# Performance work log

Hardware: AMD Instinct MI355X
Metric: run time of the kernel (lower is better)

Reference implementation:

```python
import jax, jax.numpy as jnp
import numpy as np

SEQ_LEN = 2048
EMBED = 1024
HIDDEN = 64
BATCH = 8


def setup_inputs() -> dict:
    key = jax.random.key(0)
    ks = jax.random.split(key, 7)
    s = 1.0 / np.sqrt(EMBED)
    return {
        "inputs": jax.random.normal(ks[0], (BATCH, SEQ_LEN, EMBED), dtype=jnp.float32),
        "Wq": jax.random.uniform(ks[1], (EMBED, HIDDEN), jnp.float32, -s, s),
        "bq": jax.random.uniform(ks[2], (HIDDEN,), jnp.float32, -s, s),
        "Wk": jax.random.uniform(ks[3], (EMBED, HIDDEN), jnp.float32, -s, s),
        "bk": jax.random.uniform(ks[4], (HIDDEN,), jnp.float32, -s, s),
        "Wv": jax.random.uniform(ks[5], (EMBED, HIDDEN), jnp.float32, -s, s),
        "bv": jax.random.uniform(ks[6], (HIDDEN,), jnp.float32, -s, s),
    }


def reference(inputs, Wq, bq, Wk, bk, Wv, bv):
    # inputs: [B, T, E]
    q = inputs @ Wq + bq  # [B, T, H]
    k = inputs @ Wk + bk
    v = inputs @ Wv + bv
    scale = 1.0 / jnp.sqrt(jnp.asarray(k.shape[-1], q.dtype))
    scores = jnp.einsum("bqh,bkh->bqk", q, k) * scale  # [B, T, T]
    T = scores.shape[1]
    tril = jnp.tril(jnp.ones((T, T), dtype=scores.dtype))
    # NOTE: multiplicative mask (zeros out future scores) exactly as in the torch module,
    # NOT an additive -inf mask.
    scores = scores * tril
    attn = jax.nn.softmax(scores, axis=-1)
    return jnp.einsum("bqk,bkh->bqh", attn, v)  # [B, T, H]
```

## Files before the change

### kernel.cpp

```cpp
#include <hip/hip_runtime.h>

#define NBATCH 8
#define TSEQ 2048
#define EDIM 1024
#define HDIM 64
#define NROW (NBATCH * TSEQ)

typedef unsigned short u16;
typedef __attribute__((ext_vector_type(8))) short bf16x8;
typedef __attribute__((ext_vector_type(8))) short short8;
typedef __attribute__((ext_vector_type(4))) float f32x4;

typedef unsigned int uint_as1 __attribute__((address_space(1)));
typedef unsigned int uint_as3 __attribute__((address_space(3)));

__device__ __forceinline__ u16 f2b(float x) {
  unsigned int u = __float_as_uint(x);
  unsigned int r = (u + 0x7fffu + ((u >> 16) & 1u)) >> 16;
  return (u16)r;
}
__device__ __forceinline__ float b2f(u16 h) {
  return __uint_as_float(((unsigned int)h) << 16);
}
__device__ __forceinline__ void gl16(const void* g, void* l) {
  __builtin_amdgcn_global_load_lds((const uint_as1*)g, (uint_as3*)l, 16, 0, 0);
}

__global__ __launch_bounds__(256) void wt_kernel(
    const float* __restrict__ Wq, const float* __restrict__ Wk,
    const float* __restrict__ Wv, u16* __restrict__ Wt) {
  __shared__ float s[64][65];
  const int o = blockIdx.x >> 4, et = blockIdx.x & 15;
  const float* W = (o == 0) ? Wq : (o == 1) ? Wk : Wv;
  const int t = threadIdx.x;
  const int e0 = et * 64;
#pragma unroll
  for (int i = 0; i < 16; i++) {
    int e = i * 4 + (t >> 6), h = t & 63;
    s[e][h] = W[(size_t)(e0 + e) * HDIM + h];
  }
  __syncthreads();
#pragma unroll
  for (int j = 0; j < 16; j++) {
    int h = j * 4 + (t >> 6), e = t & 63;
    Wt[(size_t)(o * 64 + h) * EDIM + e0 + e] = f2b(s[e][h]);
  }
}

#define XBUF (32 * 256)
#define WBUF (192 * 128)

__global__ __launch_bounds__(256, 2) void proj_mfma(
    const float* __restrict__ X, const u16* __restrict__ Wt,
    const float* __restrict__ bq, const float* __restrict__ bk,
    const float* __restrict__ bv,
    u16* __restrict__ Qb, u16* __restrict__ Kb, u16* __restrict__ Vt) {
  __shared__ __align__(16) char sx[2 * XBUF];
  __shared__ __align__(16) char sw[2 * WBUF];

  const int tid = threadIdx.x;
  const int w = tid >> 6, l = tid & 63;
  const int g = l >> 4, li = l & 15;
  const long bt0 = (long)blockIdx.x * 32;

  const int xr = tid >> 4, xc = tid & 15;
  const float* xsrc0 = X + (bt0 + xr) * EDIM + ((xc ^ (xr & 7)) * 4);
  const float* xsrc1 = X + (bt0 + 16 + xr) * EDIM + ((xc ^ (xr & 7)) * 4);

  f32x4 acc[6];
#pragma unroll
  for (int i = 0; i < 6; i++) acc[i] = (f32x4)0.f;

#define STAGE(BUF, E0)                                                       \
  do {                                                                       \
    gl16(xsrc0 + (E0), sx + (BUF)*XBUF + tid * 16);                          \
    gl16(xsrc1 + (E0), sx + (BUF)*XBUF + (tid + 256) * 16);                  \
    _Pragma("unroll") for (int j = 0; j < 6; j++) {                          \
      const int L = j * 256 + tid;                                           \
      const int r = L >> 3, c = L & 7;                                       \
      gl16(Wt + (size_t)r * EDIM + (E0) + ((c ^ (r & 7)) * 8),               \
           sw + (BUF)*WBUF + L * 16);                                        \
    }                                                                        \
  } while (0)

  STAGE(0, 0);
  asm volatile("s_waitcnt vmcnt(0)" ::: "memory");
  __builtin_amdgcn_sched_barrier(0);
  __builtin_amdgcn_s_barrier();
  __builtin_amdgcn_sched_barrier(0);

  for (int ks = 0; ks < 16; ks++) {
    const int buf = ks & 1;
    if (ks < 15) STAGE(buf ^ 1, (ks + 1) * 64);
    __builtin_amdgcn_sched_barrier(0);
    if (ks < 15) {
      asm volatile("s_waitcnt vmcnt(8)" ::: "memory");
    } else {
      asm volatile("s_waitcnt vmcnt(0)" ::: "memory");
    }
    __builtin_amdgcn_sched_barrier(0);
    __builtin_amdgcn_s_barrier();
    __builtin_amdgcn_sched_barrier(0);

    const char* xb = sx + buf * XBUF;
    const char* wb = sw + buf * WBUF;
    bf16x8 bfr[2][2];
#pragma unroll
    for (int cs = 0; cs < 2; cs++) {
      const int row = cs * 16 + li;
#pragma unroll
      for (int kc = 0; kc < 2; kc++) {
        const int G0 = kc * 8 + g * 2;
        const float4 f0 = *(const float4*)(xb + row * 256 + ((G0 ^ (row & 7)) * 16));
        const float4 f1 = *(const float4*)(xb + row * 256 + (((G0 + 1) ^ (row & 7)) * 16));
        bfr[cs][kc] = (bf16x8){(short)f2b(f0.x), (short)f2b(f0.y),
                               (short)f2b(f0.z), (short)f2b(f0.w),
                               (short)f2b(f1.x), (short)f2b(f1.y),
                               (short)f2b(f1.z), (short)f2b(f1.w)};
      }
    }
#pragma unroll
    for (int mt = 0; mt < 3; mt++) {
      const int row = w * 48 + mt * 16 + li;
#pragma unroll
      for (int kc = 0; kc < 2; kc++) {
        const int G = kc * 4 + g;
        const bf16x8 af = *(const bf16x8*)(wb + row * 128 + ((G ^ (row & 7)) * 16));
        acc[mt * 2 + 0] = __builtin_amdgcn_mfma_f32_16x16x32_bf16(
            af, bfr[0][kc], acc[mt * 2 + 0], 0, 0, 0);
        acc[mt * 2 + 1] = __builtin_amdgcn_mfma_f32_16x16x32_bf16(
            af, bfr[1][kc], acc[mt * 2 + 1], 0, 0, 0);
      }
    }
    __builtin_amdgcn_sched_barrier(0);
    __builtin_amdgcn_s_barrier();
    __builtin_amdgcn_sched_barrier(0);
  }
#undef STAGE

  const float qscale = 0.18033688011112042f;
#pragma unroll
  for (int cs = 0; cs < 2; cs++) {
    const long tg = bt0 + cs * 16 + li;
    const int b = (int)(tg >> 11), tl = (int)(tg & 2047);
#pragma unroll
    for (int mt = 0; mt < 3; mt++) {
      const int n0 = w * 48 + mt * 16 + g * 4;
      const int o = n0 >> 6;
      const int h0 = n0 & 63;
      const float* bias = (o == 0) ? bq : (o == 1) ? bk : bv;
      const float4 bb = *(const float4*)&bias[h0];
      const f32x4 a = acc[mt * 2 + cs];
      float v0 = a.x + bb.x, v1 = a.y + bb.y;
      float v2 = a.z + bb.z, v3 = a.w + bb.w;
      if (o == 0) {
        v0 *= qscale; v1 *= qscale; v2 *= qscale; v3 *= qscale;
        uint2 pk = make_uint2((unsigned)f2b(v0) | ((unsigned)f2b(v1) << 16),
                              (unsigned)f2b(v2) | ((unsigned)f2b(v3) << 16));
        *(uint2*)&Qb[tg * HDIM + h0] = pk;
      } else if (o == 1) {
        uint2 pk = make_uint2((unsigned)f2b(v0) | ((unsigned)f2b(v1) << 16),
                              (unsigned)f2b(v2) | ((unsigned)f2b(v3) << 16));
        *(uint2*)&Kb[tg * HDIM + h0] = pk;
      } else {
        Vt[(size_t)(b * 64 + h0 + 0) * TSEQ + tl] = f2b(v0);
        Vt[(size_t)(b * 64 + h0 + 1) * TSEQ + tl] = f2b(v1);
        Vt[(size_t)(b * 64 + h0 + 2) * TSEQ + tl] = f2b(v2);
        Vt[(size_t)(b * 64 + h0 + 3) * TSEQ + tl] = f2b(v3);
      }
    }
  }
}

__global__ __launch_bounds__(1024) void css_kernel(const u16* __restrict__ Vt,
                                                   float* __restrict__ CSS) {
  __shared__ float cs[32][64];
  const int b = blockIdx.x;
  const int t = threadIdx.x;
  const int h = t & 63, cg = t >> 6;
  const u16* vp = Vt + ((size_t)b * 64 + h) * TSEQ + cg * 128;
  float s0 = 0.f, s1 = 0.f;
#pragma unroll
  for (int i = 0; i < 8; i++) {
    const short8 a = *(const short8*)(vp + i * 8);
    s0 += b2f((u16)a[0]) + b2f((u16)a[1]) + b2f((u16)a[2]) + b2f((u16)a[3]) +
          b2f((u16)a[4]) + b2f((u16)a[5]) + b2f((u16)a[6]) + b2f((u16)a[7]);
  }
#pragma unroll
  for (int i = 8; i < 16; i++) {
    const short8 a = *(const short8*)(vp + i * 8);
    s1 += b2f((u16)a[0]) + b2f((u16)a[1]) + b2f((u16)a[2]) + b2f((u16)a[3]) +
          b2f((u16)a[4]) + b2f((u16)a[5]) + b2f((u16)a[6]) + b2f((u16)a[7]);
  }
  cs[cg * 2 + 0][h] = s0;
  cs[cg * 2 + 1][h] = s1;
  __syncthreads();
  if (t < 64) {
    float S = 0.f;
    CSS[((size_t)b * 33 + 32) * 64 + t] = 0.f;
    for (int c = 31; c >= 0; c--) {
      S += cs[c][t];
      CSS[((size_t)b * 33 + c) * 64 + t] = S;
    }
  }
}

#define ISSUE_K(K0A, K1A, KO)                                              \
  do {                                                                     \
    _Pragma("unroll") for (int n = 0; n < 4; n++) {                        \
      const u16* kp_ = Kbb + (size_t)((KO) + n * 16 + li) * HDIM + g * 8;  \
      K0A[n] = *(const bf16x8*)(kp_);                                      \
      K1A[n] = *(const bf16x8*)(kp_ + 32);                                 \
    }                                                                      \
  } while (0)

#define ISSUE_V(KO)                                                        \
  do {                                                                     \
    _Pragma("unroll") for (int n = 0; n < 4; n++) {                        \
      const u16* vp_ = Vtb + (size_t)(n * 16 + li) * TSEQ + (KO) + g * 8;  \
      vf0[n] = *(const bf16x8*)(vp_);                                      \
      vf1[n] = *(const bf16x8*)(vp_ + 32);                                 \
    }                                                                      \
  } while (0)

#define COMPUTE_TILE(K0A, K1A, KO)                                         \
  do {                                                                     \
    f32x4 sA_[4], sB_[4];                                                  \
    __builtin_amdgcn_s_setprio(1);                                         \
    _Pragma("unroll") for (int n = 0; n < 4; n++) {                        \
      sA_[n] = (f32x4)0.f;                                                 \
      sA_[n] = __builtin_amdgcn_mfma_f32_16x16x32_bf16(K0A[n], qa0[0], sA_[n], 0, 0, 0); \
      sA_[n] = __builtin_amdgcn_mfma_f32_16x16x32_bf16(K1A[n], qa0[1], sA_[n], 0, 0, 0); \
      sB_[n] = (f32x4)0.f;                                                 \
      sB_[n] = __builtin_amdgcn_mfma_f32_16x16x32_bf16(K0A[n], qa1[0], sB_[n], 0, 0, 0); \
      sB_[n] = __builtin_amdgcn_mfma_f32_16x16x32_bf16(K1A[n], qa1[1], sB_[n], 0, 0, 0); \
    }                                                                      \
    __builtin_amdgcn_s_setprio(0);                                         \
    _Pragma("unroll") for (int n = 0; n < 4; n++) {                        \
      const int kb_ = (KO) + n * 16 + g * 4;                               \
      float p0_ = (kb_ + 0 <= qiL0) ? exp2f(sA_[n][0]) : 1.0f;             \
      float p1_ = (kb_ + 1 <= qiL0) ? exp2f(sA_[n][1]) : 1.0f;             \
      float p2_ = (kb_ + 2 <= qiL0) ? exp2f(sA_[n][2]) : 1.0f;             \
      float p3_ = (kb_ + 3 <= qiL0) ? exp2f(sA_[n][3]) : 1.0f;             \
      zaccA += (p0_ + p1_) + (p2_ + p3_);                                  \
      uint2 pk_ = make_uint2((unsigned)f2b(p0_) | ((unsigned)f2b(p1_) << 16), \
                             (unsigned)f2b(p2_) | ((unsigned)f2b(p3_) << 16)); \
      *(uint2*)(sppw + li * 144 + n * 32 + g * 8) = pk_;                   \
      float q0_ = (kb_ + 0 <= qiL1) ? exp2f(sB_[n][0]) : 1.0f;             \
      float q1_ = (kb_ + 1 <= qiL1) ? exp2f(sB_[n][1]) : 1.0f;             \
      float q2_ = (kb_ + 2 <= qiL1) ? exp2f(sB_[n][2]) : 1.0f;             \
      float q3_ = (kb_ + 3 <= qiL1) ? exp2f(sB_[n][3]) : 1.0f;             \
      zaccB += (q0_ + q1_) + (q2_ + q3_);                                  \
      uint2 qk_ = make_uint2((unsigned)f2b(q0_) | ((unsigned)f2b(q1_) << 16), \
                             (unsigned)f2b(q2_) | ((unsigned)f2b(q3_) << 16)); \
      *(uint2*)(sppw + (li + 16) * 144 + n * 32 + g * 8) = qk_;            \
    }                                                                      \
    asm volatile("s_waitcnt lgkmcnt(0)" ::: "memory");                     \
    __builtin_amdgcn_sched_barrier(0);                                     \
    const bf16x8 paA0_ = *(const bf16x8*)(sppw + li * 144 + g * 16);       \
    const bf16x8 paA1_ = *(const bf16x8*)(sppw + li * 144 + 64 + g * 16);  \
    const bf16x8 paB0_ = *(const bf16x8*)(sppw + (li + 16) * 144 + g * 16);\
    const bf16x8 paB1_ = *(const bf16x8*)(sppw + (li + 16) * 144 + 64 + g * 16); \
    __builtin_amdgcn_s_setprio(1);                                         \
    _Pragma("unroll") for (int nt = 0; nt < 4; nt++) {                     \
      oaccA[nt] = __builtin_amdgcn_mfma_f32_16x16x32_bf16(paA0_, vf0[nt], oaccA[nt], 0, 0, 0); \
      oaccA[nt] = __builtin_amdgcn_mfma_f32_16x16x32_bf16(paA1_, vf1[nt], oaccA[nt], 0, 0, 0); \
      oaccB[nt] = __builtin_amdgcn_mfma_f32_16x16x32_bf16(paB0_, vf0[nt], oaccB[nt], 0, 0, 0); \
      oaccB[nt] = __builtin_amdgcn_mfma_f32_16x16x32_bf16(paB1_, vf1[nt], oaccB[nt], 0, 0, 0); \
    }                                                                      \
    __builtin_amdgcn_s_setprio(0);                                         \
  } while (0)

__global__ __launch_bounds__(256, 2) void attn_mfma(
    const u16* __restrict__ Qb, const u16* __restrict__ Kb,
    const u16* __restrict__ Vt, const float* __restrict__ CSS,
    float* __restrict__ Out) {
  __shared__ __align__(16) u16 spp[4][32][72];
  __shared__ float spm[4][32][68];

  const int tid = threadIdx.x;
  const int w = tid >> 6, l = tid & 63;
  const int g = l >> 4, li = l & 15;

  const int gb = blockIdx.x & 7;
  const int j = blockIdx.x >> 3;
  const int gr = 63 - j;
  const int q0 = gr * 32;
  const int qiL0 = q0 + li;
  const int qiL1 = q0 + 16 + li;

  char* sppw = (char*)&spp[w][0][0];

  const size_t qbase0 = ((size_t)gb * TSEQ + q0 + li) * HDIM;
  bf16x8 qa0[2], qa1[2];
  qa0[0] = *(const bf16x8*)(Qb + qbase0 + g * 8);
  qa0[1] = *(const bf16x8*)(Qb + qbase0 + g * 8 + 32);
  qa1[0] = *(const bf16x8*)(Qb + qbase0 + 16 * HDIM + g * 8);
  qa1[1] = *(const bf16x8*)(Qb + qbase0 + 16 * HDIM + g * 8 + 32);

  float zaccA = 0.f, zaccB = 0.f;
  f32x4 oaccA[4], oaccB[4];
#pragma unroll
  for (int nt = 0; nt < 4; nt++) { oaccA[nt] = (f32x4)0.f; oaccB[nt] = (f32x4)0.f; }

  const int nt = gr / 2 + 1;
  const u16* Kbb = Kb + (size_t)gb * TSEQ * HDIM;
  const u16* Vtb = Vt + (size_t)gb * 64 * TSEQ;

  bf16x8 kA0[4], kA1[4], kB0[4], kB1[4], vf0[4], vf1[4];

  int kt = w;
  if (kt < nt) {
    ISSUE_K(kA0, kA1, kt * 64);
    while (true) {
      ISSUE_V(kt * 64);
      if (kt + 4 < nt) ISSUE_K(kB0, kB1, (kt + 4) * 64);
      __builtin_amdgcn_sched_barrier(0);
      COMPUTE_TILE(kA0, kA1, kt * 64);
      kt += 4;
      if (kt >= nt) break;
      ISSUE_V(kt * 64);
      if (kt + 4 < nt) ISSUE_K(kA0, kA1, (kt + 4) * 64);
      __builtin_amdgcn_sched_barrier(0);
      COMPUTE_TILE(kB0, kB1, kt * 64);
      kt += 4;
      if (kt >= nt) break;
    }
  }

  zaccA += __shfl_xor(zaccA, 16, 64);
  zaccA += __shfl_xor(zaccA, 32, 64);
  zaccB += __shfl_xor(zaccB, 16, 64);
  zaccB += __shfl_xor(zaccB, 32, 64);

#pragma unroll
  for (int n = 0; n < 4; n++) {
#pragma unroll
    for (int r = 0; r < 4; r++) {
      spm[w][g * 4 + r][n * 16 + li] = oaccA[n][r];
      spm[w][16 + g * 4 + r][n * 16 + li] = oaccB[n][r];
    }
  }
  if (l < 16) spm[w][l][64] = zaccA;
  else if (l < 32) spm[w][16 + (l & 15)][64] = zaccB;
  __syncthreads();

  const float tailz = (float)(TSEQ - nt * 64);
  const float tailv = CSS[((size_t)gb * 33 + nt) * 64 + l];
#pragma unroll
  for (int r = 0; r < 8; r++) {
    const int q = w * 8 + r;
    const int qi = q0 + q;
    float a = ((spm[0][q][l] + spm[1][q][l]) + (spm[2][q][l] + spm[3][q][l]));
    float zz = ((spm[0][q][64] + spm[1][q][64]) + (spm[2][q][64] + spm[3][q][64]));
    zz += tailz;
    a += tailv;
    Out[((size_t)gb * TSEQ + qi) * HDIM + l] = a / zz;
  }
}

extern "C" void kernel_launch(void* const* d_in, const int* in_sizes, int n_in,
                              void* d_out, int out_size, void* d_ws, size_t ws_size,
                              hipStream_t stream) {
  const float* X  = (const float*)d_in[0];
  const float* Wq = (const float*)d_in[1];
  const float* bq = (const float*)d_in[2];
  const float* Wk = (const float*)d_in[3];
  const float* bk = (const float*)d_in[4];
  const float* Wv = (const float*)d_in[5];
  const float* bv = (const float*)d_in[6];
  float* out = (float*)d_out;

  char* ws = (char*)d_ws;
  u16*   Qb  = (u16*)(ws);
  u16*   Kb  = (u16*)(ws + 2097152);
  u16*   Vt  = (u16*)(ws + 4194304);
  u16*   Wt  = (u16*)(ws + 6291456);
  float* CSS = (float*)(ws + 6684672);

  wt_kernel<<<48, 256, 0, stream>>>(Wq, Wk, Wv, Wt);
  proj_mfma<<<NROW / 32, 256, 0, stream>>>(X, Wt, bq, bk, bv, Qb, Kb, Vt);
  css_kernel<<<NBATCH, 1024, 0, stream>>>(Vt, CSS);
  attn_mfma<<<512, 256, 0, stream>>>(Qb, Kb, Vt, CSS, out);
}
```

Before: 69.71 us.

## Split projection kernel across Q/K/V outputs to triple grid parallelism

The projection kernel now launches three times as many blocks, and each block computes only one of the Q, K or V outputs (64 columns) for its 32-row tile. This shrinks the weight LDS buffer, the per-block accumulators and the number of loads per stage. The launch bound rises to 4 blocks per CU for higher occupancy. In exchange, each fp32 input tile is read from global memory three times and converted to bf16 three times, which triples the dominant X traffic unless L2 absorbs it.

```diff
diff --git a/kernel.cpp b/kernel.cpp
--- a/kernel.cpp
+++ b/kernel.cpp
@@ -48,9 +48,9 @@
 }
 
 #define XBUF (32 * 256)
-#define WBUF (192 * 128)
-
-__global__ __launch_bounds__(256, 2) void proj_mfma(
+#define WBUF (64 * 128)
+
+__global__ __launch_bounds__(256, 4) void proj_mfma(
     const float* __restrict__ X, const u16* __restrict__ Wt,
     const float* __restrict__ bq, const float* __restrict__ bk,
     const float* __restrict__ bv,
@@ -61,24 +61,26 @@
   const int tid = threadIdx.x;
   const int w = tid >> 6, l = tid & 63;
   const int g = l >> 4, li = l & 15;
-  const long bt0 = (long)blockIdx.x * 32;
+  const int o = blockIdx.x % 3;
+  const long bt0 = (long)(blockIdx.x / 3) * 32;
 
   const int xr = tid >> 4, xc = tid & 15;
   const float* xsrc0 = X + (bt0 + xr) * EDIM + ((xc ^ (xr & 7)) * 4);
   const float* xsrc1 = X + (bt0 + 16 + xr) * EDIM + ((xc ^ (xr & 7)) * 4);
-
-  f32x4 acc[6];
-#pragma unroll
-  for (int i = 0; i < 6; i++) acc[i] = (f32x4)0.f;
+  const u16* wsrc = Wt + (size_t)o * 64 * EDIM;
+
+  f32x4 acc[2];
+  acc[0] = (f32x4)0.f;
+  acc[1] = (f32x4)0.f;
 
 #define STAGE(BUF, E0)                                                       \
   do {                                                                       \
     gl16(xsrc0 + (E0), sx + (BUF)*XBUF + tid * 16);                          \
     gl16(xsrc1 + (E0), sx + (BUF)*XBUF + (tid + 256) * 16);                  \
-    _Pragma("unroll") for (int j = 0; j < 6; j++) {                          \
+    _Pragma("unroll") for (int j = 0; j < 2; j++) {                          \
       const int L = j * 256 + tid;                                           \
       const int r = L >> 3, c = L & 7;                                       \
-      gl16(Wt + (size_t)r * EDIM + (E0) + ((c ^ (r & 7)) * 8),               \
+      gl16(wsrc + (size_t)r * EDIM + (E0) + ((c ^ (r & 7)) * 8),             \
            sw + (BUF)*WBUF + L * 16);                                        \
     }                                                                        \
   } while (0)
@@ -94,7 +96,7 @@
     if (ks < 15) STAGE(buf ^ 1, (ks + 1) * 64);
     __builtin_amdgcn_sched_barrier(0);
     if (ks < 15) {
-      asm volatile("s_waitcnt vmcnt(8)" ::: "memory");
+      asm volatile("s_waitcnt vmcnt(4)" ::: "memory");
     } else {
       asm volatile("s_waitcnt vmcnt(0)" ::: "memory");
     }
@@ -119,17 +121,14 @@
                                (short)f2b(f1.z), (short)f2b(f1.w)};
       }
     }
-#pragma unroll
-    for (int mt = 0; mt < 3; mt++) {
-      const int row = w * 48 + mt * 16 + li;
+    {
+      const int row = w * 16 + li;
 #pragma unroll
       for (int kc = 0; kc < 2; kc++) {
         const int G = kc * 4 + g;
         const bf16x8 af = *(const bf16x8*)(wb + row * 128 + ((G ^ (row & 7)) * 16));
-        acc[mt * 2 + 0] = __builtin_amdgcn_mfma_f32_16x16x32_bf16(
-            af, bfr[0][kc], acc[mt * 2 + 0], 0, 0, 0);
-        acc[mt * 2 + 1] = __builtin_amdgcn_mfma_f32_16x16x32_bf16(
-            af, bfr[1][kc], acc[mt * 2 + 1], 0, 0, 0);
+        acc[0] = __builtin_amdgcn_mfma_f32_16x16x32_bf16(af, bfr[0][kc], acc[0], 0, 0, 0);
+        acc[1] = __builtin_amdgcn_mfma_f32_16x16x32_bf16(af, bfr[1][kc], acc[1], 0, 0, 0);
       }
     }
     __builtin_amdgcn_sched_barrier(0);
@@ -139,35 +138,30 @@
 #undef STAGE
 
   const float qscale = 0.18033688011112042f;
+  const int h0 = w * 16 + g * 4;
+  const float* bias = (o == 0) ? bq : (o == 1) ? bk : bv;
+  const float4 bb = *(const float4*)&bias[h0];
 #pragma unroll
   for (int cs = 0; cs < 2; cs++) {
     const long tg = bt0 + cs * 16 + li;
     const int b = (int)(tg >> 11), tl = (int)(tg & 2047);
-#pragma unroll
-    for (int mt = 0; mt < 3; mt++) {
-      const int n0 = w * 48 + mt * 16 + g * 4;
-      const int o = n0 >> 6;
-      const int h0 = n0 & 63;
-      const float* bias = (o == 0) ? bq : (o == 1) ? bk : bv;
-      const float4 bb = *(const float4*)&bias[h0];
-      const f32x4 a = acc[mt * 2 + cs];
-      float v0 = a.x + bb.x, v1 = a.y + bb.y;
-      float v2 = a.z + bb.z, v3 = a.w + bb.w;
-      if (o == 0) {
-        v0 *= qscale; v1 *= qscale; v2 *= qscale; v3 *= qscale;
-        uint2 pk = make_uint2((unsigned)f2b(v0) | ((unsigned)f2b(v1) << 16),
-                              (unsigned)f2b(v2) | ((unsigned)f2b(v3) << 16));
-        *(uint2*)&Qb[tg * HDIM + h0] = pk;
-      } else if (o == 1) {
-        uint2 pk = make_uint2((unsigned)f2b(v0) | ((unsigned)f2b(v1) << 16),
-                              (unsigned)f2b(v2) | ((unsigned)f2b(v3) << 16));
-        *(uint2*)&Kb[tg * HDIM + h0] = pk;
-      } else {
-        Vt[(size_t)(b * 64 + h0 + 0) * TSEQ + tl] = f2b(v0);
-        Vt[(size_t)(b * 64 + h0 + 1) * TSEQ + tl] = f2b(v1);
-        Vt[(size_t)(b * 64 + h0 + 2) * TSEQ + tl] = f2b(v2);
-        Vt[(size_t)(b * 64 + h0 + 3) * TSEQ + tl] = f2b(v3);
-      }
+    const f32x4 a = acc[cs];
+    float v0 = a.x + bb.x, v1 = a.y + bb.y;
+    float v2 = a.z + bb.z, v3 = a.w + bb.w;
+    if (o == 0) {
+      v0 *= qscale; v1 *= qscale; v2 *= qscale; v3 *= qscale;
+      uint2 pk = make_uint2((unsigned)f2b(v0) | ((unsigned)f2b(v1) << 16),
+                            (unsigned)f2b(v2) | ((unsigned)f2b(v3) << 16));
+      *(uint2*)&Qb[tg * HDIM + h0] = pk;
+    } else if (o == 1) {
+      uint2 pk = make_uint2((unsigned)f2b(v0) | ((unsigned)f2b(v1) << 16),
+                            (unsigned)f2b(v2) | ((unsigned)f2b(v3) << 16));
+      *(uint2*)&Kb[tg * HDIM + h0] = pk;
+    } else {
+      Vt[(size_t)(b * 64 + h0 + 0) * TSEQ + tl] = f2b(v0);
+      Vt[(size_t)(b * 64 + h0 + 1) * TSEQ + tl] = f2b(v1);
+      Vt[(size_t)(b * 64 + h0 + 2) * TSEQ + tl] = f2b(v2);
+      Vt[(size_t)(b * 64 + h0 + 3) * TSEQ + tl] = f2b(v3);
     }
   }
 }
@@ -379,7 +373,7 @@
   float* CSS = (float*)(ws + 6684672);
 
   wt_kernel<<<48, 256, 0, stream>>>(Wq, Wk, Wv, Wt);
-  proj_mfma<<<NROW / 32, 256, 0, stream>>>(X, Wt, bq, bk, bv, Qb, Kb, Vt);
+  proj_mfma<<<(NROW / 32) * 3, 256, 0, stream>>>(X, Wt, bq, bk, bv, Qb, Kb, Vt);
   css_kernel<<<NBATCH, 1024, 0, stream>>>(Vt, CSS);
   attn_mfma<<<512, 256, 0, stream>>>(Qb, Kb, Vt, CSS, out);
 }
```

Measured after the change: 83.12 us. 1.19x slower.
